# Performance work log

Measured on AMD Instinct MI355X. Metric: run time of the kernel, lower is better.

The kernel has to match this reference:

```python
import jax, jax.numpy as jnp
import numpy as np

BITS = 8
QMAX = float(2 ** (BITS - 1) - 1)   # 127
QMIN = -float(2 ** (BITS - 1))      # -128
LORA_SCALING = 2.0                  # alpha=16 / r=8


def fake_quant(x):
    """Per-tensor symmetric fake quantization with STE (STE irrelevant for fwd)."""
    scale = jnp.maximum(jnp.max(jnp.abs(x)) / QMAX, 1e-8)
    y = jnp.clip(jnp.round(x / scale), QMIN, QMAX) * scale
    return x + jax.lax.stop_gradient(y - x)


def qat_linear_lora(x, W, b, A, B):
    # fake-quantized main path + full-precision LoRA path
    xq = fake_quant(x)
    Wq = fake_quant(W)
    main = jnp.einsum('bsi,oi->bso', xq, Wq) + b
    lora = jnp.einsum('bsr,or->bso', jnp.einsum('bsi,ri->bsr', x, A), B) * LORA_SCALING
    return main + lora


def setup_inputs() -> dict:
    key = jax.random.key(0)
    ks = jax.random.split(key, 6)
    n_embd, d_ff, r = 1024, 4096, 8
    B_, S = 4, 2048
    return {
        'hidden_states': jax.random.normal(ks[0], (B_, S, n_embd), jnp.float32),
        'W_fc': jax.random.normal(ks[1], (d_ff, n_embd), jnp.float32) * 0.02,
        'b_fc': jnp.zeros((d_ff,), jnp.float32),
        'A_fc': jax.random.normal(ks[2], (r, n_embd), jnp.float32) * (1.0 / n_embd) ** 0.5,
        'B_fc': jnp.zeros((d_ff, r), jnp.float32),
        'W_proj': jax.random.normal(ks[3], (n_embd, d_ff), jnp.float32) * 0.02,
        'b_proj': jnp.zeros((n_embd,), jnp.float32),
        'A_proj': jax.random.normal(ks[4], (r, d_ff), jnp.float32) * (1.0 / d_ff) ** 0.5,
        'B_proj': jnp.zeros((n_embd, r), jnp.float32),
    }


def reference(hidden_states, W_fc, b_fc, A_fc, B_fc, W_proj, b_proj, A_proj, B_proj):
    h = qat_linear_lora(hidden_states, W_fc, b_fc, A_fc, B_fc)
    h = jax.nn.gelu(h, approximate=False)  # nn.GELU() default = exact erf GELU
    h = qat_linear_lora(h, W_proj, b_proj, A_proj, B_proj)
    return h
```

## Files before the change

kernel.cpp:

```cpp
#include <hip/hip_runtime.h>
#include <hip/hip_bf16.h>
#include <hip/hip_fp16.h>
#include <math.h>


typedef unsigned short u16;
typedef unsigned int u32;
typedef signed char i8;
typedef int i32x4 __attribute__((ext_vector_type(4)));
typedef _Float16 f16;
typedef f16 f16x8 __attribute__((ext_vector_type(8)));
typedef float f32x4 __attribute__((ext_vector_type(4)));

#define ASYNC16(gp, lp)                                                        \
  __builtin_amdgcn_global_load_lds(                                            \
      (__attribute__((address_space(1))) void*)(gp),                           \
      (__attribute__((address_space(3))) void*)(lp), 16, 0, 0)

#define VMCNT(N) asm volatile("s_waitcnt vmcnt(" #N ")" ::: "memory")
#define LGKM0 asm volatile("s_waitcnt lgkmcnt(0)" ::: "memory")
#define SBAR __builtin_amdgcn_s_barrier()

__device__ __forceinline__ int quanti(float v, float inv) {
  float q = rintf(v * inv);
  q = fminf(fmaxf(q, -128.0f), 127.0f);
  return (int)q;
}

__device__ __forceinline__ u32 pack4(float4 v, float inv) {
  return ((u32)(quanti(v.x, inv) & 255)) |
         ((u32)(quanti(v.y, inv) & 255) << 8) |
         ((u32)(quanti(v.z, inv) & 255) << 16) |
         ((u32)(quanti(v.w, inv) & 255) << 24);
}

__device__ __forceinline__ float load_scale(const u32* slot) {
  return fmaxf(__uint_as_float(*slot) * (1.0f / 127.0f), 1e-8f);
}

__device__ __forceinline__ float gelu_erf(float v) {
  float z = fabsf(v) * 0.70710678118654752f;
  float t = __builtin_amdgcn_rcpf(fmaf(0.3275911f, z, 1.0f));
  float poly =
      t * fmaf(t,
               fmaf(t,
                    fmaf(t, fmaf(t, 1.061405429f, -1.453152027f),
                         1.421413741f),
                    -0.284496736f),
               0.254829592f);
  float e = fmaf(-poly, exp2f(-z * z * 1.4426950408889634f), 1.0f);
  return 0.5f * v * fmaf(copysignf(e, v), 1.0f, 1.0f);
}

__global__ void absmax_kernel(const float* __restrict__ x, int n4,
                              u32* __restrict__ slot) {
  float m = 0.0f;
  int stride = gridDim.x * blockDim.x;
  for (int i = blockIdx.x * blockDim.x + threadIdx.x; i < n4; i += stride) {
    float4 v = ((const float4*)x)[i];
    m = fmaxf(m, fmaxf(fmaxf(fabsf(v.x), fabsf(v.y)),
                       fmaxf(fabsf(v.z), fabsf(v.w))));
  }
#pragma unroll
  for (int off = 32; off > 0; off >>= 1) m = fmaxf(m, __shfl_down(m, off));
  __shared__ float wmax[4];
  int lane = threadIdx.x & 63, wave = threadIdx.x >> 6;
  if (lane == 0) wmax[wave] = m;
  __syncthreads();
  if (threadIdx.x == 0) {
    m = fmaxf(fmaxf(wmax[0], wmax[1]), fmaxf(wmax[2], wmax[3]));
    atomicMax(slot, __float_as_uint(m));
  }
}

__global__ void quant_w_kernel(const float* __restrict__ w, int n16,
                               const u32* __restrict__ slot,
                               i8* __restrict__ q) {
  float inv = 1.0f / load_scale(slot);
  int stride = gridDim.x * blockDim.x;
  for (int i = blockIdx.x * blockDim.x + threadIdx.x; i < n16; i += stride) {
    const float4* src = (const float4*)w + i * 4;
    u32 pk[4];
#pragma unroll
    for (int c = 0; c < 4; c++) pk[c] = pack4(src[c], inv);
    uint4 o = {pk[0], pk[1], pk[2], pk[3]};
    ((uint4*)q)[i] = o;
  }
}

__global__ void conv_a16_kernel(const float* __restrict__ A,
                                f16* __restrict__ Ah, int ncols) {
  int i = blockIdx.x * blockDim.x + threadIdx.x;
  int base = i * 8;
  if (base >= 16 * ncols) return;
  if (base < 8 * ncols) {
    float4 v0 = ((const float4*)(A + base))[0];
    float4 v1 = ((const float4*)(A + base))[1];
    f16x8 o = {(f16)v0.x, (f16)v0.y, (f16)v0.z, (f16)v0.w,
               (f16)v1.x, (f16)v1.y, (f16)v1.z, (f16)v1.w};
    *(f16x8*)(Ah + base) = o;
  } else {
    f16x8 z = {};
    *(f16x8*)(Ah + base) = z;
  }
}

__launch_bounds__(256) __global__
    void quant_x_t1_fused(const float* __restrict__ x,
                          const f16* __restrict__ Ah,
                          const u32* __restrict__ slot,
                          i8* __restrict__ xq,
                          float* __restrict__ t1) {
  int tid = threadIdx.x;
  int lane = tid & 63, wave = tid >> 6;
  int quad = lane >> 4, l15 = lane & 15;
  int bx = blockIdx.x;
  long m0 = (long)blockIdx.y * 64 + wave * 16;
  long row = m0 + l15;
  int k0 = bx * 512;
  float inv = 1.0f / load_scale(slot);

  const float* xp = x + row * 1024 + k0 + quad * 8;
  const f16* ap = Ah + l15 * 1024 + k0 + quad * 8;
  i8* op = xq + row * 1024 + k0 + quad * 8;
  f32x4 acc = {0.0f, 0.0f, 0.0f, 0.0f};
#pragma unroll
  for (int s = 0; s < 16; s++) {
    float4 v0 = ((const float4*)(xp + s * 32))[0];
    float4 v1 = ((const float4*)(xp + s * 32))[1];
    f16x8 af = {(f16)v0.x, (f16)v0.y, (f16)v0.z, (f16)v0.w,
                (f16)v1.x, (f16)v1.y, (f16)v1.z, (f16)v1.w};
    f16x8 bf = *(const f16x8*)(ap + s * 32);
    acc = __builtin_amdgcn_mfma_f32_16x16x32_f16(af, bf, acc, 0, 0, 0);
    uint2 o = {pack4(v0, inv), pack4(v1, inv)};
    *(uint2*)(op + s * 32) = o;
  }
  if (l15 < 8) {
#pragma unroll
    for (int r = 0; r < 4; r++) {
      long m = m0 + quad * 4 + r;
      atomicAdd(&t1[m * 8 + l15], acc[r]);
    }
  }
}

__launch_bounds__(256) __global__
    void quant_h_t2_fused(u16* __restrict__ h,
                          const f16* __restrict__ Ah,
                          const u32* __restrict__ slot,
                          float* __restrict__ t2) {
  int tid = threadIdx.x;
  int lane = tid & 63, wave = tid >> 6;
  int quad = lane >> 4, l15 = lane & 15;
  int bx = blockIdx.x;
  long m0 = (long)blockIdx.y * 64 + wave * 16;
  long row = m0 + l15;
  int k0 = bx * 512;
  float inv = 1.0f / load_scale(slot);

  const u16* hp = h + row * 4096 + k0 + quad * 8;
  const f16* ap = Ah + l15 * 4096 + k0 + quad * 8;
  f32x4 acc = {0.0f, 0.0f, 0.0f, 0.0f};
  u32 q[32];
#pragma unroll
  for (int s = 0; s < 16; s++) {
    uint4 hv = *(const uint4*)(hp + s * 32);
    f16x8 af = *(const f16x8*)&hv;
    f16x8 bf = *(const f16x8*)(ap + s * 32);
    acc = __builtin_amdgcn_mfma_f32_16x16x32_f16(af, bf, acc, 0, 0, 0);
    u32 uu[4] = {hv.x, hv.y, hv.z, hv.w};
#pragma unroll
    for (int c = 0; c < 2; c++) {
      float2 f0 = __half22float2(*(__half2*)&uu[2 * c]);
      float2 f1 = __half22float2(*(__half2*)&uu[2 * c + 1]);
      q[2 * s + c] = ((u32)(quanti(f0.x, inv) & 255)) |
                     ((u32)(quanti(f0.y, inv) & 255) << 8) |
                     ((u32)(quanti(f1.x, inv) & 255) << 16) |
                     ((u32)(quanti(f1.y, inv) & 255) << 24);
    }
  }
  asm volatile("" ::: "memory");
  i8* op = (i8*)h + row * 8192 + bx * 1024 + quad * 8;
#pragma unroll
  for (int s = 0; s < 16; s++) {
    uint2 o = {q[2 * s], q[2 * s + 1]};
    *(uint2*)(op + s * 32) = o;
  }
  if (l15 < 8) {
#pragma unroll
    for (int r = 0; r < 4; r++) {
      long m = m0 + quad * 4 + r;
      atomicAdd(&t2[m * 8 + l15], acc[r]);
    }
  }
}

template <int MODE>
__launch_bounds__(256, 2) __global__
    void gemm4w_kernel(const i8* __restrict__ A, const i8* __restrict__ B,
                       int N, int K, int lda, int ldb,
                       const float* __restrict__ bias,
                       const float* __restrict__ tl,
                       const float* __restrict__ Bl,
                       const u32* __restrict__ scales, int sa, int sb,
                       void* __restrict__ outp, u32* __restrict__ hmax) {
  constexpr int MT = 4, NT = 4;
  __shared__ __align__(16) i8 As[2][128 * 128];
  __shared__ __align__(16) i8 Bs[2][128 * 128];
  __shared__ u32 bmax;
  int tid = threadIdx.x;
  int lane = tid & 63, wave = tid >> 6;
  int quad = lane >> 4, l15 = lane & 15;
  int wm = (wave & 1) * 64, wn = (wave >> 1) * 64;
  int nwg = gridDim.x * gridDim.y;
  int lin = blockIdx.y * gridDim.x + blockIdx.x;
  int swb = (lin & 7) * (nwg >> 3) + (lin >> 3);
  int bx = swb % gridDim.x, by = swb / gridDim.x;
  long m0 = (long)by * 128;
  long n0 = (long)bx * 128;
  if (MODE == 0 && tid == 0) bmax = 0u;

  const i8* pA[2];
  const i8* pB[2];
  int ldsOff[2];
#pragma unroll
  for (int u = 0; u < 2; u++) {
    int c = u * 256 + tid;
    int row = c >> 3;
    int swz = ((c & 7) ^ (row & 7)) * 16;
    pA[u] = A + (m0 + row) * lda + swz;
    pB[u] = B + (n0 + row) * ldb + swz;
    ldsOff[u] = c * 16;
  }

  auto stageA = [&](int t, int h) {
    int kb = (MODE == 1) ? ((t >> 2) * 1024 + (t & 3) * 128) : (t << 7);
#pragma unroll
    for (int u = 0; u < 2; u++)
      ASYNC16(pA[u] + (long)h * 64 * lda + kb,
              &As[t & 1][h * 8192 + ldsOff[u]]);
  };
  auto stageB = [&](int t, int h) {
    int kb = t << 7;
#pragma unroll
    for (int u = 0; u < 2; u++)
      ASYNC16(pB[u] + (long)h * 64 * ldb + kb,
              &Bs[t & 1][h * 8192 + ldsOff[u]]);
  };

  int s0 = (quad ^ (l15 & 7)) * 16;
  int s1 = s0 ^ 64;

  i32x4 acc[MT][NT] = {};
  int NTILES = K >> 7;

  stageA(0, 0); stageA(0, 1); stageB(0, 0); stageB(0, 1);
  stageA(1, 0); stageA(1, 1);
  VMCNT(4);
  SBAR;

  for (int t = 0; t < NTILES; t++) {
    const i8* Ab = As[t & 1];
    const i8* Bb = Bs[t & 1];
    i32x4 a0[MT], a1[MT], b0[NT], b1[NT];
#pragma unroll
    for (int i = 0; i < MT; i++) {
      a0[i] = *(const i32x4*)(Ab + (wm + i * 16 + l15) * 128 + s0);
      a1[i] = *(const i32x4*)(Ab + (wm + i * 16 + l15) * 128 + s1);
    }
#pragma unroll
    for (int j = 0; j < NT; j++)
      b0[j] = *(const i32x4*)(Bb + (wn + j * 16 + l15) * 128 + s0);
    if (t + 1 < NTILES) { stageB(t + 1, 0); stageB(t + 1, 1); }
    SBAR;
    LGKM0;
    __builtin_amdgcn_s_setprio(1);
#pragma unroll
    for (int i = 0; i < MT; i++)
#pragma unroll
      for (int j = 0; j < NT; j++)
        acc[i][j] = __builtin_amdgcn_mfma_i32_16x16x64_i8(a0[i], b0[j],
                                                          acc[i][j], 0, 0, 0);
    __builtin_amdgcn_s_setprio(0);
    SBAR;
#pragma unroll
    for (int j = 0; j < NT; j++)
      b1[j] = *(const i32x4*)(Bb + (wn + j * 16 + l15) * 128 + s1);
    if (t + 2 < NTILES) { stageA(t + 2, 0); stageA(t + 2, 1); }
    SBAR;
    LGKM0;
    __builtin_amdgcn_s_setprio(1);
#pragma unroll
    for (int i = 0; i < MT; i++)
#pragma unroll
      for (int j = 0; j < NT; j++)
        acc[i][j] = __builtin_amdgcn_mfma_i32_16x16x64_i8(a1[i], b1[j],
                                                          acc[i][j], 0, 0, 0);
    __builtin_amdgcn_s_setprio(0);
    if (t + 2 < NTILES) {
      VMCNT(4);
    } else {
      VMCNT(0);
    }
    SBAR;
  }

  float scale = load_scale(scales + sa) * load_scale(scales + sb);
  float biasv[NT];
  float4 bl0[NT], bl1[NT];
#pragma unroll
  for (int j = 0; j < NT; j++) {
    long n = n0 + wn + j * 16 + l15;
    biasv[j] = bias[n];
    bl0[j] = ((const float4*)(Bl + n * 8))[0];
    bl1[j] = ((const float4*)(Bl + n * 8))[1];
  }
  float lmax = 0.0f;
#pragma unroll
  for (int i = 0; i < MT; i++) {
#pragma unroll
    for (int r = 0; r < 4; r++) {
      long m = m0 + wm + i * 16 + quad * 4 + r;
      float4 t0 = ((const float4*)(tl + m * 8))[0];
      float4 t1v = ((const float4*)(tl + m * 8))[1];
#pragma unroll
      for (int j = 0; j < NT; j++) {
        long n = n0 + wn + j * 16 + l15;
        float lora = t0.x * bl0[j].x + t0.y * bl0[j].y + t0.z * bl0[j].z +
                     t0.w * bl0[j].w + t1v.x * bl1[j].x + t1v.y * bl1[j].y +
                     t1v.z * bl1[j].z + t1v.w * bl1[j].w;
        float v = (float)acc[i][j][r] * scale + biasv[j] + 2.0f * lora;
        if (MODE == 0) {
          float hv = gelu_erf(v);
          __half hh = __float2half_rn(hv);
          ((u16*)outp)[m * N + n] = *(u16*)&hh;
          lmax = fmaxf(lmax, fabsf(hv));
        } else {
          ((float*)outp)[m * N + n] = v;
        }
      }
    }
  }
  if (MODE == 0) {
    atomicMax(&bmax, __float_as_uint(lmax));
    __syncthreads();
    if (tid == 0) atomicMax(hmax, bmax);
  }
}

extern "C" void kernel_launch(void* const* d_in, const int* in_sizes, int n_in,
                              void* d_out, int out_size, void* d_ws,
                              size_t ws_size, hipStream_t stream) {
  const float* x = (const float*)d_in[0];
  const float* Wfc = (const float*)d_in[1];
  const float* bfc = (const float*)d_in[2];
  const float* Afc = (const float*)d_in[3];
  const float* Bfc = (const float*)d_in[4];
  const float* Wpr = (const float*)d_in[5];
  const float* bpr = (const float*)d_in[6];
  const float* Apr = (const float*)d_in[7];
  const float* Bpr = (const float*)d_in[8];
  float* out = (float*)d_out;

  char* w = (char*)d_ws;
  u32* scales = (u32*)w;
  float* t1 = (float*)(w + 256);
  float* t2 = (float*)(w + 256 + 262144);
  i8* xq = (i8*)(w + 524544);
  f16* aprh = (f16*)(w + 8913152);
  f16* afch = (f16*)(w + 9175040);
  i8* wq1 = (i8*)(w + 9437184);
  i8* wq2 = (i8*)(w + 13631488);
  u16* hq = (u16*)(w + 17825792);
  if (ws_size < 84934656) return;

  hipMemsetAsync(w, 0, 524544, stream);
  conv_a16_kernel<<<32, 256, 0, stream>>>(Apr, aprh, 4096);
  conv_a16_kernel<<<8, 256, 0, stream>>>(Afc, afch, 1024);
  absmax_kernel<<<1024, 256, 0, stream>>>(x, 8192 * 1024 / 4, scales + 0);
  absmax_kernel<<<512, 256, 0, stream>>>(Wfc, 4096 * 1024 / 4, scales + 1);
  absmax_kernel<<<512, 256, 0, stream>>>(Wpr, 4096 * 1024 / 4, scales + 2);
  quant_x_t1_fused<<<dim3(2, 128), 256, 0, stream>>>(x, afch, scales + 0, xq,
                                                     t1);
  quant_w_kernel<<<256, 256, 0, stream>>>(Wfc, 4096 * 1024 / 16, scales + 1,
                                          wq1);
  quant_w_kernel<<<256, 256, 0, stream>>>(Wpr, 4096 * 1024 / 16, scales + 2,
                                          wq2);
  gemm4w_kernel<0><<<dim3(32, 64), 256, 0, stream>>>(
      xq, wq1, 4096, 1024, 1024, 1024, bfc, t1, Bfc, scales, 0, 1, hq,
      scales + 3);
  quant_h_t2_fused<<<dim3(8, 128), 256, 0, stream>>>(hq, aprh, scales + 3, t2);
  gemm4w_kernel<1><<<dim3(8, 64), 256, 0, stream>>>(
      (const i8*)hq, wq2, 1024, 4096, 8192, 4096, bpr, t2, Bpr, scales, 3, 2,
      out, nullptr);
}
```

Before: 304.7 us.

## Load GEMM A operand directly into registers, stage only B through LDS

The int8 GEMM stops staging the A tile through shared memory. Each wave now loads its A fragments straight from global memory into registers, double-buffered one tile ahead, while B is still staged asynchronously into LDS. This halves LDS footprint and LDS traffic and merges the two half-K phases into one body with a single barrier per tile. In exchange each lane issues uncoalesced 16-byte global reads (one row per lane), A data shared between waves is fetched redundantly, and register pressure rises. The loop also waits with vmcnt(0) every iteration and steps two tiles at a time, assuming an even tile count.

New measurement: 374.3 us. 1.23x slower.

```diff
diff --git a/kernel.cpp b/kernel.cpp
--- a/kernel.cpp
+++ b/kernel.cpp
@@ -17,8 +17,7 @@
       (__attribute__((address_space(1))) void*)(gp),                           \
       (__attribute__((address_space(3))) void*)(lp), 16, 0, 0)
 
-#define VMCNT(N) asm volatile("s_waitcnt vmcnt(" #N ")" ::: "memory")
-#define LGKM0 asm volatile("s_waitcnt lgkmcnt(0)" ::: "memory")
+#define VMCNT0 asm volatile("s_waitcnt vmcnt(0)" ::: "memory")
 #define SBAR __builtin_amdgcn_s_barrier()
 
 __device__ __forceinline__ int quanti(float v, float inv) {
@@ -197,7 +196,7 @@
 
 template <int MODE>
 __launch_bounds__(256, 2) __global__
-    void gemm4w_kernel(const i8* __restrict__ A, const i8* __restrict__ B,
+    void gemmra_kernel(const i8* __restrict__ A, const i8* __restrict__ B,
                        int N, int K, int lda, int ldb,
                        const float* __restrict__ bias,
                        const float* __restrict__ tl,
@@ -205,7 +204,6 @@
                        const u32* __restrict__ scales, int sa, int sb,
                        void* __restrict__ outp, u32* __restrict__ hmax) {
   constexpr int MT = 4, NT = 4;
-  __shared__ __align__(16) i8 As[2][128 * 128];
   __shared__ __align__(16) i8 Bs[2][128 * 128];
   __shared__ u32 bmax;
   int tid = threadIdx.x;
@@ -220,32 +218,36 @@
   long n0 = (long)bx * 128;
   if (MODE == 0 && tid == 0) bmax = 0u;
 
-  const i8* pA[2];
-  const i8* pB[2];
-  int ldsOff[2];
-#pragma unroll
-  for (int u = 0; u < 2; u++) {
+  const i8* pB[4];
+  int ldsB[4];
+#pragma unroll
+  for (int u = 0; u < 4; u++) {
     int c = u * 256 + tid;
     int row = c >> 3;
     int swz = ((c & 7) ^ (row & 7)) * 16;
-    pA[u] = A + (m0 + row) * lda + swz;
     pB[u] = B + (n0 + row) * ldb + swz;
-    ldsOff[u] = c * 16;
-  }
-
-  auto stageA = [&](int t, int h) {
-    int kb = (MODE == 1) ? ((t >> 2) * 1024 + (t & 3) * 128) : (t << 7);
-#pragma unroll
-    for (int u = 0; u < 2; u++)
-      ASYNC16(pA[u] + (long)h * 64 * lda + kb,
-              &As[t & 1][h * 8192 + ldsOff[u]]);
+    ldsB[u] = c * 16;
+  }
+  auto stageB = [&](int t) {
+    int kb = t << 7;
+#pragma unroll
+    for (int u = 0; u < 4; u++) ASYNC16(pB[u] + kb, &Bs[t & 1][ldsB[u]]);
   };
-  auto stageB = [&](int t, int h) {
-    int kb = t << 7;
-#pragma unroll
-    for (int u = 0; u < 2; u++)
-      ASYNC16(pB[u] + (long)h * 64 * ldb + kb,
-              &Bs[t & 1][h * 8192 + ldsOff[u]]);
+
+  const i8* rowA[MT];
+#pragma unroll
+  for (int i = 0; i < MT; i++)
+    rowA[i] = A + (m0 + wm + i * 16 + l15) * (long)lda + quad * 16;
+  auto koff = [&](int t) -> int {
+    return (MODE == 1) ? ((t >> 2) * 1024 + (t & 3) * 128) : (t << 7);
+  };
+  auto loadA = [&](int t, i32x4 (&ar)[MT][2]) {
+    int kb = koff(t);
+#pragma unroll
+    for (int i = 0; i < MT; i++) {
+      ar[i][0] = *(const i32x4*)(rowA[i] + kb);
+      ar[i][1] = *(const i32x4*)(rowA[i] + kb + 64);
+    }
   };
 
   int s0 = (quad ^ (l15 & 7)) * 16;
@@ -254,55 +256,42 @@
   i32x4 acc[MT][NT] = {};
   int NTILES = K >> 7;
 
-  stageA(0, 0); stageA(0, 1); stageB(0, 0); stageB(0, 1);
-  stageA(1, 0); stageA(1, 1);
-  VMCNT(4);
-  SBAR;
-
-  for (int t = 0; t < NTILES; t++) {
-    const i8* Ab = As[t & 1];
+  auto body = [&](int t, i32x4 (&cur)[MT][2], i32x4 (&nxt)[MT][2]) {
+    if (t + 1 < NTILES) loadA(t + 1, nxt);
+    i32x4 b0[NT], b1[NT];
     const i8* Bb = Bs[t & 1];
-    i32x4 a0[MT], a1[MT], b0[NT], b1[NT];
-#pragma unroll
-    for (int i = 0; i < MT; i++) {
-      a0[i] = *(const i32x4*)(Ab + (wm + i * 16 + l15) * 128 + s0);
-      a1[i] = *(const i32x4*)(Ab + (wm + i * 16 + l15) * 128 + s1);
-    }
-#pragma unroll
-    for (int j = 0; j < NT; j++)
+#pragma unroll
+    for (int j = 0; j < NT; j++) {
       b0[j] = *(const i32x4*)(Bb + (wn + j * 16 + l15) * 128 + s0);
-    if (t + 1 < NTILES) { stageB(t + 1, 0); stageB(t + 1, 1); }
-    SBAR;
-    LGKM0;
+      b1[j] = *(const i32x4*)(Bb + (wn + j * 16 + l15) * 128 + s1);
+    }
+    if (t + 1 < NTILES) stageB(t + 1);
     __builtin_amdgcn_s_setprio(1);
 #pragma unroll
     for (int i = 0; i < MT; i++)
 #pragma unroll
       for (int j = 0; j < NT; j++)
-        acc[i][j] = __builtin_amdgcn_mfma_i32_16x16x64_i8(a0[i], b0[j],
+        acc[i][j] = __builtin_amdgcn_mfma_i32_16x16x64_i8(cur[i][0], b0[j],
+                                                          acc[i][j], 0, 0, 0);
+#pragma unroll
+    for (int i = 0; i < MT; i++)
+#pragma unroll
+      for (int j = 0; j < NT; j++)
+        acc[i][j] = __builtin_amdgcn_mfma_i32_16x16x64_i8(cur[i][1], b1[j],
                                                           acc[i][j], 0, 0, 0);
     __builtin_amdgcn_s_setprio(0);
+    VMCNT0;
     SBAR;
-#pragma unroll
-    for (int j = 0; j < NT; j++)
-      b1[j] = *(const i32x4*)(Bb + (wn + j * 16 + l15) * 128 + s1);
-    if (t + 2 < NTILES) { stageA(t + 2, 0); stageA(t + 2, 1); }
-    SBAR;
-    LGKM0;
-    __builtin_amdgcn_s_setprio(1);
-#pragma unroll
-    for (int i = 0; i < MT; i++)
-#pragma unroll
-      for (int j = 0; j < NT; j++)
-        acc[i][j] = __builtin_amdgcn_mfma_i32_16x16x64_i8(a1[i], b1[j],
-                                                          acc[i][j], 0, 0, 0);
-    __builtin_amdgcn_s_setprio(0);
-    if (t + 2 < NTILES) {
-      VMCNT(4);
-    } else {
-      VMCNT(0);
-    }
-    SBAR;
+  };
+
+  i32x4 aP[MT][2], aN[MT][2];
+  loadA(0, aP);
+  stageB(0);
+  VMCNT0;
+  SBAR;
+  for (int t = 0; t < NTILES; t += 2) {
+    body(t, aP, aN);
+    body(t + 1, aN, aP);
   }
 
   float scale = load_scale(scales + sa) * load_scale(scales + sb);
@@ -386,11 +375,11 @@
                                           wq1);
   quant_w_kernel<<<256, 256, 0, stream>>>(Wpr, 4096 * 1024 / 16, scales + 2,
                                           wq2);
-  gemm4w_kernel<0><<<dim3(32, 64), 256, 0, stream>>>(
+  gemmra_kernel<0><<<dim3(32, 64), 256, 0, stream>>>(
       xq, wq1, 4096, 1024, 1024, 1024, bfc, t1, Bfc, scales, 0, 1, hq,
       scales + 3);
   quant_h_t2_fused<<<dim3(8, 128), 256, 0, stream>>>(hq, aprh, scales + 3, t2);
-  gemm4w_kernel<1><<<dim3(8, 64), 256, 0, stream>>>(
+  gemmra_kernel<1><<<dim3(8, 64), 256, 0, stream>>>(
       (const i8*)hq, wq2, 1024, 4096, 8192, 4096, bpr, t2, Bpr, scales, 3, 2,
       out, nullptr);
 }
```
